# Kernel optimization log

Measured on AMD Instinct MI355X. Metric: run time of the kernel, lower is better.

Reference implementation:

```python
import jax, jax.numpy as jnp
import numpy as np

H = 16            # num_attention_heads
START_RATIO = 0.1
RECENT_RATIO = 0.4
THETA = 10000.0
CHUNK = 256       # hard-coded chunk_size in source
CLIP = 1e4        # nan_to_num posinf/neginf bound


def _rope_cos_sin(T, D, dtype):
    inv_freq = 1.0 / (THETA ** (jnp.arange(0, D, 2, dtype=jnp.float32) / D))
    freqs = jnp.arange(T, dtype=jnp.float32)[:, None] * inv_freq[None, :]  # [T, D/2]
    emb = jnp.concatenate([freqs, freqs], axis=-1)                          # [T, D]
    return jnp.cos(emb).astype(dtype), jnp.sin(emb).astype(dtype)


def _apply_rope(x, cos, sin):
    # x: [B,H,T,D]; cos/sin: [T,D] broadcast over B,H
    d = x.shape[-1] // 2
    rot = jnp.concatenate([-x[..., d:], x[..., :d]], axis=-1)
    return x * cos + rot * sin


def setup_inputs() -> dict:
    key = jax.random.key(0)
    k0, k1, k2, k3, k4 = jax.random.split(key, 5)
    B, T, Dm = 1, 2048, 2048
    scale = 1.0 / np.sqrt(Dm).astype(np.float32)
    return {
        "hidden_states": jax.random.normal(k0, (B, T, Dm), jnp.float32),
        "Wq": jax.random.normal(k1, (Dm, Dm), jnp.float32) * scale,
        "Wk": jax.random.normal(k2, (Dm, Dm), jnp.float32) * scale,
        "Wv": jax.random.normal(k3, (Dm, Dm), jnp.float32) * scale,
        "Wo": jax.random.normal(k4, (Dm, Dm), jnp.float32) * scale,
    }


def reference(hidden_states, Wq, Wk, Wv, Wo):
    B, T, Dm = hidden_states.shape
    D = Dm // H
    hs = jnp.nan_to_num(hidden_states, nan=0.0, posinf=CLIP, neginf=-CLIP)

    def proj(W):  # torch Linear: x @ W.T, then [B,T,H,D] -> [B,H,T,D]
        return (hs @ W.T).reshape(B, T, H, D).transpose(0, 2, 1, 3)

    q, k, v = proj(Wq), proj(Wk), proj(Wv)
    cos, sin = _rope_cos_sin(T, D, hs.dtype)
    q = _apply_rope(q, cos, sin)
    k = _apply_rope(k, cos, sin)

    # start+recent keep mask (past_key_value=None -> k_len == T)
    k_len = T
    sb = max(0, min(int(START_RATIO * k_len), k_len))
    rb = max(0, min(int(RECENT_RATIO * k_len), k_len - sb))
    pos = jnp.arange(k_len)
    keep = (pos < sb) | (pos >= k_len - rb)          # [K]

    MIN = jnp.finfo(hs.dtype).min
    scores = jnp.einsum('bhqd,bhkd->bhqk', q, k) / jnp.sqrt(jnp.asarray(D, hs.dtype))
    scores = jnp.where(keep, scores, MIN)
    probs = jax.nn.softmax(scores, axis=-1)          # [B,H,T,K]

    # CaM merge of evicted V into recent window, driven by the LAST query row.
    evict = k_len - rb                               # static python int
    last = probs[..., -1, :]                         # [B,H,K]
    mean_attn = last[..., evict + 1:].mean(axis=-1) + 1e-6
    p = jnp.clip(last[..., evict] / mean_attn, 0.0, 1.0)
    p = jnp.nan_to_num(p, nan=0.0, posinf=1.0, neginf=0.0)
    u = jax.random.uniform(jax.random.key(42), p.shape, p.dtype)
    bern = (u < p).astype(v.dtype)                   # [B,H]
    v_e = v[..., evict, :] * bern[..., None] / rb    # [B,H,D]
    v_merged = v.at[..., evict + 1:, :].add(v_e[..., None, :])

    # Chunked loop effect: only the last chunk's AV uses merged V.
    last_start = ((T - 1) // CHUNK) * CHUNK
    out_pre = jnp.einsum('bhqk,bhkd->bhqd', probs[:, :, :last_start], v)
    out_last = jnp.einsum('bhqk,bhkd->bhqd', probs[:, :, last_start:], v_merged)
    out = jnp.concatenate([out_pre, out_last], axis=2)   # [B,H,T,D]

    out = out.transpose(0, 2, 1, 3).reshape(B, T, Dm) @ Wo.T
    return jnp.nan_to_num(out, nan=0.0, posinf=CLIP, neginf=-CLIP)
```

## Files before the change

kernel.cpp:

```cpp
#include <hip/hip_runtime.h>
#include <stdint.h>

#define T_SEQ 2048
#define DM    2048
#define NH    16
#define HD    128
#define SB    204
#define EV    1229
#define RB    819
#define NRECF 818.0f
#define LAST_START 1792
#define SCALE 0.08838834764831845f

typedef __attribute__((ext_vector_type(8))) short short8;
typedef __attribute__((ext_vector_type(4))) short short4v;
typedef __attribute__((ext_vector_type(4))) float f32x4;

__device__ __forceinline__ unsigned short f2bf(float f) {
  uint32_t u = __float_as_uint(f);
  u += 0x7fffu + ((u >> 16) & 1u);
  return (unsigned short)(u >> 16);
}
__device__ __forceinline__ float bf2f(unsigned short s) {
  return __uint_as_float(((uint32_t)s) << 16);
}
__device__ __forceinline__ void gload16(const void* g, void* l) {
  __builtin_amdgcn_global_load_lds((const __attribute__((address_space(1))) void*)g,
                                   (__attribute__((address_space(3))) void*)l,
                                   16, 0, 0);
}
__device__ __forceinline__ float n2n(float v) {
  if (isnan(v)) return 0.0f;
  if (isinf(v)) return v > 0.0f ? 10000.0f : -10000.0f;
  return v;
}

__global__ __launch_bounds__(256) void cvt_kernel(
    const float* __restrict__ hs, const float* __restrict__ wq,
    const float* __restrict__ wk, const float* __restrict__ wv,
    const float* __restrict__ wo, unsigned short* __restrict__ hsb,
    unsigned short* __restrict__ wqb, unsigned short* __restrict__ wkb,
    unsigned short* __restrict__ wvb, unsigned short* __restrict__ wob,
    float* __restrict__ cst, float* __restrict__ snt) {
  if (blockIdx.x >= 20480) {
    int idx = (blockIdx.x - 20480) * 256 + threadIdx.x;
    int t = idx >> 6, i = idx & 63;
    float inv = (float)exp(-(double)i * log(10000.0) / 64.0);
    float ang = (float)t * inv;
    cst[idx] = (float)cos((double)ang);
    snt[idx] = (float)sin((double)ang);
    return;
  }
  int gid = blockIdx.x * 256 + threadIdx.x;
  int region = gid >> 20;
  int off4 = (gid & 1048575) * 4;
  const float* src; unsigned short* dst;
  switch (region) {
    case 0: src = hs; dst = hsb; break;
    case 1: src = wq; dst = wqb; break;
    case 2: src = wk; dst = wkb; break;
    case 3: src = wv; dst = wvb; break;
    default: src = wo; dst = wob; break;
  }
  float4 v = *(const float4*)(src + off4);
  if (region == 0) { v.x = n2n(v.x); v.y = n2n(v.y); v.z = n2n(v.z); v.w = n2n(v.w); }
  ushort4 o;
  o.x = f2bf(v.x); o.y = f2bf(v.y); o.z = f2bf(v.z); o.w = f2bf(v.w);
  *(ushort4*)(dst + off4) = o;
}

__device__ __forceinline__ void gemm_mainloop64_db(
    const unsigned short* __restrict__ A, const unsigned short* __restrict__ B,
    unsigned short* LDSBUF,
    int m0, int n0, int k0, int ksteps, int tid, f32x4 (&acc)[4][4]) {
  int w = tid >> 6, lane = tid & 63;
  int wm = w >> 1, wn = w & 1;
  int q4 = lane >> 4, r = lane & 15;
  f32x4 zero = {0.f, 0.f, 0.f, 0.f};
  #pragma unroll
  for (int mi = 0; mi < 4; mi++)
    #pragma unroll
    for (int ni = 0; ni < 4; ni++) acc[mi][ni] = zero;
  int srow = w * 32 + (lane >> 3);
  int swz = ((lane & 7) ^ (lane >> 3)) * 16;
  const char* Ag = (const char*)(A + (size_t)(m0 + srow) * DM) + swz + k0 * 2;
  const char* Bg = (const char*)(B + (size_t)(n0 + srow) * DM) + swz + k0 * 2;
  unsigned short* AsB[2] = {LDSBUF + w * 2048, LDSBUF + 16384 + w * 2048};
  unsigned short* BsB[2] = {LDSBUF + 8192 + w * 2048, LDSBUF + 24576 + w * 2048};
  #pragma unroll
  for (int g = 0; g < 4; g++) {
    gload16(Ag + g * (8 * DM * 2), AsB[0] + g * 512);
    gload16(Bg + g * (8 * DM * 2), BsB[0] + g * 512);
  }
  for (int s = 0; s < ksteps; s++) {
    int db = s & 1;
    __syncthreads();
    if (s + 1 < ksteps) {
      #pragma unroll
      for (int g = 0; g < 4; g++) {
        gload16(Ag + 128 + g * (8 * DM * 2), AsB[db ^ 1] + g * 512);
        gload16(Bg + 128 + g * (8 * DM * 2), BsB[db ^ 1] + g * 512);
      }
    }
    Ag += 128; Bg += 128;
    const unsigned short* As = LDSBUF + (db ? 16384 : 0);
    const unsigned short* Bs = LDSBUF + (db ? 24576 : 8192);
    #pragma unroll
    for (int kh = 0; kh < 2; kh++) {
      int pcs = ((kh * 4 + q4) ^ (r & 7)) * 8;
      short8 a[4], b[4];
      #pragma unroll
      for (int mi = 0; mi < 4; mi++)
        a[mi] = *(const short8*)(As + (wm * 64 + mi * 16 + r) * 64 + pcs);
      #pragma unroll
      for (int ni = 0; ni < 4; ni++)
        b[ni] = *(const short8*)(Bs + ((ni & 1) * 64 + wn * 32 + (ni >> 1) * 16 + r) * 64 + pcs);
      #pragma unroll
      for (int mi = 0; mi < 4; mi++)
        #pragma unroll
        for (int ni = 0; ni < 4; ni++)
          acc[mi][ni] = __builtin_amdgcn_mfma_f32_16x16x32_bf16(a[mi], b[ni], acc[mi][ni], 0, 0, 0);
    }
  }
}

__global__ __launch_bounds__(256, 2) void gemm_qkv_kernel(
    const unsigned short* __restrict__ hsb, const unsigned short* __restrict__ wqb,
    const unsigned short* __restrict__ wkb, const unsigned short* __restrict__ wvb,
    const float* __restrict__ cst, const float* __restrict__ snt,
    unsigned short* __restrict__ qbf, unsigned short* __restrict__ kbf,
    unsigned short* __restrict__ vbT) {
  __shared__ __align__(16) unsigned short LDSBUF[32768];
  int z = blockIdx.z;
  const unsigned short* B = (z == 0) ? wqb : (z == 1) ? wkb : wvb;
  int m0 = blockIdx.y * 128, n0 = blockIdx.x * 128;
  f32x4 acc[4][4];
  gemm_mainloop64_db(hsb, B, LDSBUF, m0, n0, 0, DM / 64, threadIdx.x, acc);
  int tid = threadIdx.x, w = tid >> 6, lane = tid & 63;
  int wm = w >> 1, wn = w & 1, q4 = lane >> 4, r = lane & 15;
  int h = n0 >> 7;
  if (z < 2) {
    unsigned short* dst = (z == 0) ? qbf : kbf;
    #pragma unroll
    for (int mi = 0; mi < 4; mi++)
      #pragma unroll
      for (int p = 0; p < 2; p++) {
        int d = wn * 32 + p * 16 + r;
        #pragma unroll
        for (int g = 0; g < 4; g++) {
          int t = m0 + wm * 64 + mi * 16 + q4 * 4 + g;
          float c = cst[t * 64 + d], s = snt[t * 64 + d];
          float x0 = acc[mi][2 * p][g], x1 = acc[mi][2 * p + 1][g];
          dst[((size_t)h * T_SEQ + t) * HD + d]      = f2bf(x0 * c - x1 * s);
          dst[((size_t)h * T_SEQ + t) * HD + d + 64] = f2bf(x1 * c + x0 * s);
        }
      }
  } else {
    __syncthreads();
    #pragma unroll
    for (int mi = 0; mi < 4; mi++)
      #pragma unroll
      for (int ni = 0; ni < 4; ni++) {
        int c = (ni & 1) * 64 + wn * 32 + (ni >> 1) * 16 + r;
        int tl = wm * 64 + mi * 16 + q4 * 4;
        short4v pv;
        pv[0] = (short)f2bf(acc[mi][ni][0]);
        pv[1] = (short)f2bf(acc[mi][ni][1]);
        pv[2] = (short)f2bf(acc[mi][ni][2]);
        pv[3] = (short)f2bf(acc[mi][ni][3]);
        *(short4v*)(LDSBUF + c * 136 + tl) = pv;
      }
    __syncthreads();
    int d = tid >> 1, th = tid & 1;
    unsigned short* gdst = vbT + ((size_t)h * HD + d) * T_SEQ + m0 + th * 64;
    const unsigned short* lsrc = LDSBUF + d * 136 + th * 64;
    #pragma unroll
    for (int j = 0; j < 8; j++)
      *(short8*)(gdst + j * 8) = *(const short8*)(lsrc + j * 8);
  }
}

__device__ __forceinline__ void attn_body(
    int kb, const unsigned short* Kt, const unsigned short* Vt,
    const unsigned short* indv, unsigned short* Psw,
    const short8 (&aq)[4], f32x4 (&o)[8], f32x4& o9, float (&evf)[4],
    int q4, int r) {
  f32x4 zero = {0.f, 0.f, 0.f, 0.f};
  int rsw = (r >> 1) & 3;
  f32x4 s0 = zero, s1 = zero;
  #pragma unroll
  for (int c = 0; c < 4; c++) {
    int pc = ((c * 4 + q4) ^ r) * 8;
    short8 bk0 = *(const short8*)(Kt + r * 128 + pc);
    short8 bk1 = *(const short8*)(Kt + (16 + r) * 128 + pc);
    s0 = __builtin_amdgcn_mfma_f32_16x16x32_bf16(aq[c], bk0, s0, 0, 0, 0);
    s1 = __builtin_amdgcn_mfma_f32_16x16x32_bf16(aq[c], bk1, s1, 0, 0, 0);
  }
  int kg0 = kb + r, kg1 = kb + 16 + r;
  bool keep0 = (kg0 < SB) || (kg0 >= EV);
  bool keep1 = (kg1 < SB) || (kg1 >= EV);
  #pragma unroll
  for (int g = 0; g < 4; g++) {
    float p0 = keep0 ? __expf(fmaf(s0[g], SCALE, -8.0f)) : 0.0f;
    float p1 = keep1 ? __expf(fmaf(s1[g], SCALE, -8.0f)) : 0.0f;
    if (kb == 1216 && kg0 == EV) evf[g] = p0;
    int row = q4 * 4 + g;
    int psw = (row >> 1) & 3;
    Psw[row * 32 + (((r >> 3) ^ psw) * 8) + (r & 7)]       = f2bf(p0);
    Psw[row * 32 + ((((r >> 3) + 2) ^ psw) * 8) + (r & 7)] = f2bf(p1);
  }
  short8 pa = *(const short8*)(Psw + r * 32 + (q4 ^ rsw) * 8);
  #pragma unroll
  for (int ni = 0; ni < 8; ni++) {
    short8 bv = *(const short8*)(Vt + (ni * 16 + r) * 32 + (q4 ^ rsw) * 8);
    o[ni] = __builtin_amdgcn_mfma_f32_16x16x32_bf16(pa, bv, o[ni], 0, 0, 0);
  }
  short8 bind = *(const short8*)(indv + r * 32 + (q4 ^ rsw) * 8);
  o9 = __builtin_amdgcn_mfma_f32_16x16x32_bf16(pa, bind, o9, 0, 0, 0);
}

__global__ __launch_bounds__(256, 2) void attn_kernel(
    const unsigned short* __restrict__ qbf, const unsigned short* __restrict__ kbf,
    const unsigned short* __restrict__ vbT, unsigned short* __restrict__ atb,
    float* __restrict__ attnf_s, float* __restrict__ Ssum, float* __restrict__ lst) {
  __shared__ __align__(16) unsigned short KtS[2][2][4096];
  __shared__ __align__(16) unsigned short VtS[2][2][4096];
  __shared__ __align__(16) unsigned short Ps[4][512];
  __shared__ __align__(16) unsigned short Ind[3 * 512];
  int tid = threadIdx.x, w = tid >> 6, lane = tid & 63;
  int q4 = lane >> 4, r = lane & 15;
  int h = blockIdx.y;
  int qb = blockIdx.x * 64 + w * 16;

  for (int idx = tid; idx < 3 * 512; idx += 256) {
    int v = idx >> 9, n = (idx >> 5) & 15, j = idx & 31;
    float val = 0.f;
    if (n == 0) val = 1.f;
    else if (n == 1) val = (v == 1) ? (j >= 14 ? 1.f : 0.f) : (v == 2 ? 1.f : 0.f);
    Ind[v * 512 + n * 32 + (((j >> 3) ^ ((n >> 1) & 3)) * 8) + (j & 7)] = f2bf(val);
  }

  short8 aq[4];
  {
    const unsigned short* qrow = qbf + ((size_t)h * T_SEQ + qb + r) * HD;
    #pragma unroll
    for (int c = 0; c < 4; c++) aq[c] = *(const short8*)(qrow + c * 32 + q4 * 8);
  }
  f32x4 zero = {0.f, 0.f, 0.f, 0.f};
  f32x4 o[8], o9;
  #pragma unroll
  for (int ni = 0; ni < 8; ni++) o[ni] = zero;
  o9 = zero;
  float evf[4] = {0.f, 0.f, 0.f, 0.f};

  const char* Kbase = (const char*)(kbf + (size_t)h * T_SEQ * HD);
  int krow0 = w * 8 + q4, krow1 = krow0 + 4;
  const char* Kg0 = Kbase + krow0 * 256 + ((r ^ (krow0 & 15)) * 16);
  const char* Kg1 = Kbase + krow1 * 256 + ((r ^ (krow1 & 15)) * 16);
  const char* Vbase = (const char*)(vbT + (size_t)h * HD * T_SEQ);
  int vsrc = ((lane & 3) ^ ((lane >> 3) & 3)) * 16;
  const char* Vg0 = Vbase + (size_t)(w * 32 + (lane >> 2)) * 4096 + vsrc;
  const char* Vg1 = Vg0 + 16 * 4096;

  auto issue_chunk = [&](int ci, int db) {
    int kb = (ci < 4) ? ci * 64 : 1216 + (ci - 4) * 64;
    gload16(Kg0 + kb * 256,         &KtS[db][0][w * 1024]);
    gload16(Kg1 + kb * 256,         &KtS[db][0][w * 1024 + 512]);
    gload16(Kg0 + (kb + 32) * 256,  &KtS[db][1][w * 1024]);
    gload16(Kg1 + (kb + 32) * 256,  &KtS[db][1][w * 1024 + 512]);
    gload16(Vg0 + kb * 2,           &VtS[db][0][w * 1024]);
    gload16(Vg1 + kb * 2,           &VtS[db][0][w * 1024 + 512]);
    gload16(Vg0 + (kb + 32) * 2,    &VtS[db][1][w * 1024]);
    gload16(Vg1 + (kb + 32) * 2,    &VtS[db][1][w * 1024 + 512]);
  };

  issue_chunk(0, 0);
  for (int ci = 0; ci < 17; ci++) {
    int db = ci & 1;
    int kb = (ci < 4) ? ci * 64 : 1216 + (ci - 4) * 64;
    const unsigned short* indA = Ind + ((ci < 4) ? 0 : (ci == 4) ? 512 : 1024);
    const unsigned short* indB = Ind + ((ci < 4) ? 0 : 1024);
    __syncthreads();
    if (ci < 16) issue_chunk(ci + 1, db ^ 1);
    attn_body(kb,      KtS[db][0], VtS[db][0], indA, &Ps[w][0], aq, o, o9, evf, q4, r);
    attn_body(kb + 32, KtS[db][1], VtS[db][1], indB, &Ps[w][0], aq, o, o9, evf, q4, r);
  }

  float invl[4], srn[4], evn[4];
  #pragma unroll
  for (int g = 0; g < 4; g++) {
    float l  = __shfl(o9[g], lane & 48, 64);
    float sr = __shfl(o9[g], (lane & 48) | 1, 64);
    float ev = __shfl(evf[g], (lane & 48) | 13, 64);
    invl[g] = 1.0f / l;
    srn[g] = sr * invl[g];
    evn[g] = ev * invl[g];
  }
  if (blockIdx.x < (LAST_START / 64)) {
    #pragma unroll
    for (int ni = 0; ni < 8; ni++)
      #pragma unroll
      for (int g = 0; g < 4; g++)
        atb[(size_t)(qb + q4 * 4 + g) * DM + h * HD + ni * 16 + r] = f2bf(o[ni][g] * invl[g]);
  } else {
    #pragma unroll
    for (int ni = 0; ni < 8; ni++)
      #pragma unroll
      for (int g = 0; g < 4; g++)
        attnf_s[(size_t)(qb - LAST_START + q4 * 4 + g) * DM + h * HD + ni * 16 + r] = o[ni][g] * invl[g];
  }
  if (r == 0) {
    #pragma unroll
    for (int g = 0; g < 4; g++) {
      int t = qb + q4 * 4 + g;
      if (t >= LAST_START) Ssum[h * 256 + (t - LAST_START)] = srn[g];
      if (t == T_SEQ - 1) { lst[h * 2] = evn[g]; lst[h * 2 + 1] = srn[g]; }
    }
  }
}

__device__ __forceinline__ void tf_round(uint32_t& x0, uint32_t& x1, int rot) {
  x0 += x1;
  x1 = (x1 << rot) | (x1 >> (32 - rot));
  x1 ^= x0;
}
__device__ __forceinline__ float bern_scale(int hh, const float* lst) {
  const uint32_t k0 = 0u, k1 = 42u, k2 = 0x1BD11BDAu ^ k0 ^ k1;
  uint32_t x0 = (uint32_t)(hh & 7), x1 = (uint32_t)((hh & 7) + 8);
  x0 += k0; x1 += k1;
  tf_round(x0, x1, 13); tf_round(x0, x1, 15); tf_round(x0, x1, 26); tf_round(x0, x1, 6);
  x0 += k1; x1 += k2 + 1u;
  tf_round(x0, x1, 17); tf_round(x0, x1, 29); tf_round(x0, x1, 16); tf_round(x0, x1, 24);
  x0 += k2; x1 += k0 + 2u;
  tf_round(x0, x1, 13); tf_round(x0, x1, 15); tf_round(x0, x1, 26); tf_round(x0, x1, 6);
  x0 += k0; x1 += k1 + 3u;
  tf_round(x0, x1, 17); tf_round(x0, x1, 29); tf_round(x0, x1, 16); tf_round(x0, x1, 24);
  x0 += k1; x1 += k2 + 4u;
  tf_round(x0, x1, 13); tf_round(x0, x1, 15); tf_round(x0, x1, 26); tf_round(x0, x1, 6);
  x0 += k2; x1 += k0 + 5u;
  uint32_t bits = (hh < 8) ? x0 : x1;
  float u = __uint_as_float((bits >> 9) | 0x3f800000u) - 1.0f;
  float evp = lst[hh * 2], srp = lst[hh * 2 + 1];
  float mean = srp * (1.0f / NRECF) + 1e-6f;
  float p = evp / mean;
  p = fminf(fmaxf(p, 0.0f), 1.0f);
  if (!(p == p)) p = 0.0f;
  return (u < p) ? (1.0f / (float)RB) : 0.0f;
}

__global__ __launch_bounds__(256) void fixup_kernel(
    const float* __restrict__ attnf_s, const float* __restrict__ Ssum,
    const float* __restrict__ lst, const unsigned short* __restrict__ vbT,
    unsigned short* __restrict__ atb) {
  int idx = blockIdx.x * 256 + threadIdx.x;
  int t2 = idx >> 11, n = idx & 2047;
  int h = n >> 7, d = n & 127;
  float bsc = bern_scale(h, lst);
  float v = attnf_s[idx];
  v += Ssum[h * 256 + t2] * bsc * bf2f(vbT[((size_t)h * HD + d) * T_SEQ + EV]);
  atb[(size_t)(t2 + LAST_START) * DM + n] = f2bf(v);
}

__global__ __launch_bounds__(256, 2) void gemm_out_kernel(
    const unsigned short* __restrict__ atb, const unsigned short* __restrict__ wob,
    float* __restrict__ part0, float* __restrict__ part1) {
  __shared__ __align__(16) unsigned short LDSBUF[32768];
  int m0 = blockIdx.y * 128, n0 = blockIdx.x * 128;
  int kz = blockIdx.z;
  float* part = kz ? part1 : part0;
  f32x4 acc[4][4];
  gemm_mainloop64_db(atb, wob, LDSBUF, m0, n0, kz * 1024, 16, threadIdx.x, acc);
  int tid = threadIdx.x, w = tid >> 6, lane = tid & 63;
  int wm = w >> 1, wn = w & 1, q4 = lane >> 4, r = lane & 15;
  #pragma unroll
  for (int mi = 0; mi < 4; mi++)
    #pragma unroll
    for (int ni = 0; ni < 4; ni++) {
      int c = n0 + (ni & 1) * 64 + wn * 32 + (ni >> 1) * 16 + r;
      #pragma unroll
      for (int g = 0; g < 4; g++) {
        int t = m0 + wm * 64 + mi * 16 + q4 * 4 + g;
        part[(size_t)t * DM + c] = acc[mi][ni][g];
      }
    }
}

__global__ __launch_bounds__(256) void add_kernel(
    const float* __restrict__ p0, const float* __restrict__ p1, float* __restrict__ out) {
  int i4 = (blockIdx.x * 256 + threadIdx.x) * 4;
  float4 a = *(const float4*)(p0 + i4);
  float4 b = *(const float4*)(p1 + i4);
  float4 o;
  o.x = n2n(a.x + b.x); o.y = n2n(a.y + b.y);
  o.z = n2n(a.z + b.z); o.w = n2n(a.w + b.w);
  *(float4*)(out + i4) = o;
}

extern "C" void kernel_launch(void* const* d_in, const int* in_sizes, int n_in,
                              void* d_out, int out_size, void* d_ws, size_t ws_size,
                              hipStream_t stream) {
  const float* hs = (const float*)d_in[0];
  const float* Wq = (const float*)d_in[1];
  const float* Wk = (const float*)d_in[2];
  const float* Wv = (const float*)d_in[3];
  const float* Wo = (const float*)d_in[4];
  char* ws = (char*)d_ws;
  const size_t MB = 1024 * 1024;
  unsigned short* hsb = (unsigned short*)(ws + 0);
  unsigned short* wqb = (unsigned short*)(ws + 8 * MB);
  unsigned short* wkb = (unsigned short*)(ws + 16 * MB);
  unsigned short* wvb = (unsigned short*)(ws + 24 * MB);
  unsigned short* wob = (unsigned short*)(ws + 32 * MB);
  unsigned short* qbf = (unsigned short*)(ws + 40 * MB);
  unsigned short* kbf = (unsigned short*)(ws + 48 * MB);
  unsigned short* vbT = (unsigned short*)(ws + 56 * MB);
  unsigned short* atb = (unsigned short*)(ws + 64 * MB);
  float* attnf_s = (float*)(ws + 72 * MB);
  float* part0 = (float*)(ws + 74 * MB);
  float* part1 = (float*)(ws + 90 * MB);
  float* cst = (float*)(ws + 106 * MB);
  float* snt = (float*)(ws + 106 * MB + 524288);
  float* Ssum = (float*)(ws + 107 * MB);
  float* lst = (float*)(ws + 107 * MB + 16384);

  cvt_kernel<<<20992, 256, 0, stream>>>(hs, Wq, Wk, Wv, Wo, hsb, wqb, wkb, wvb, wob, cst, snt);
  gemm_qkv_kernel<<<dim3(16, 16, 3), 256, 0, stream>>>(hsb, wqb, wkb, wvb, cst, snt, qbf, kbf, vbT);
  attn_kernel<<<dim3(32, 16), 256, 0, stream>>>(qbf, kbf, vbT, atb, attnf_s, Ssum, lst);
  fixup_kernel<<<2048, 256, 0, stream>>>(attnf_s, Ssum, lst, vbT, atb);
  gemm_out_kernel<<<dim3(16, 16, 2), 256, 0, stream>>>(atb, wob, part0, part1);
  add_kernel<<<4096, 256, 0, stream>>>(part0, part1, (float*)d_out);
}
```

Measured before the change: 248.2 us.

## Skip K/V projection rows for evicted keys and single-buffer GEMM LDS

The QKV projection grid now computes only the K and V row tiles that the start+recent mask can touch (the first 2 and the last 7 of 16 tiles), while Q keeps all 16. This cuts about a third of the projection GEMM work. Both GEMMs also drop LDS double-buffering in favour of one buffer with two barriers per k-step. That halves LDS use so launch bounds can allow three blocks per CU, at the cost of losing load/compute overlap inside a block. The skipped K/V rows are left unwritten, so this relies on the attention kernel never reading them, including the evict row 1229, which falls in tile 9.

Result: faster. 242.5 us (-2.3%).

```diff
diff --git a/kernel.cpp b/kernel.cpp
--- a/kernel.cpp
+++ b/kernel.cpp
@@ -69,10 +69,10 @@
   *(ushort4*)(dst + off4) = o;
 }
 
-__device__ __forceinline__ void gemm_mainloop64_db(
+__device__ __forceinline__ void gemm_mainloop64(
     const unsigned short* __restrict__ A, const unsigned short* __restrict__ B,
-    unsigned short* LDSBUF,
-    int m0, int n0, int k0, int ksteps, int tid, f32x4 (&acc)[4][4]) {
+    unsigned short* As, unsigned short* Bs, int m0, int n0, int k0, int ksteps,
+    int tid, f32x4 (&acc)[4][4]) {
   int w = tid >> 6, lane = tid & 63;
   int wm = w >> 1, wn = w & 1;
   int q4 = lane >> 4, r = lane & 15;
@@ -85,26 +85,17 @@
   int swz = ((lane & 7) ^ (lane >> 3)) * 16;
   const char* Ag = (const char*)(A + (size_t)(m0 + srow) * DM) + swz + k0 * 2;
   const char* Bg = (const char*)(B + (size_t)(n0 + srow) * DM) + swz + k0 * 2;
-  unsigned short* AsB[2] = {LDSBUF + w * 2048, LDSBUF + 16384 + w * 2048};
-  unsigned short* BsB[2] = {LDSBUF + 8192 + w * 2048, LDSBUF + 24576 + w * 2048};
-  #pragma unroll
-  for (int g = 0; g < 4; g++) {
-    gload16(Ag + g * (8 * DM * 2), AsB[0] + g * 512);
-    gload16(Bg + g * (8 * DM * 2), BsB[0] + g * 512);
-  }
+  unsigned short* Asl = As + w * 2048;
+  unsigned short* Bsl = Bs + w * 2048;
   for (int s = 0; s < ksteps; s++) {
-    int db = s & 1;
     __syncthreads();
-    if (s + 1 < ksteps) {
-      #pragma unroll
-      for (int g = 0; g < 4; g++) {
-        gload16(Ag + 128 + g * (8 * DM * 2), AsB[db ^ 1] + g * 512);
-        gload16(Bg + 128 + g * (8 * DM * 2), BsB[db ^ 1] + g * 512);
-      }
+    #pragma unroll
+    for (int g = 0; g < 4; g++) {
+      gload16(Ag + g * (8 * DM * 2), Asl + g * 512);
+      gload16(Bg + g * (8 * DM * 2), Bsl + g * 512);
     }
     Ag += 128; Bg += 128;
-    const unsigned short* As = LDSBUF + (db ? 16384 : 0);
-    const unsigned short* Bs = LDSBUF + (db ? 24576 : 8192);
+    __syncthreads();
     #pragma unroll
     for (int kh = 0; kh < 2; kh++) {
       int pcs = ((kh * 4 + q4) ^ (r & 7)) * 8;
@@ -124,33 +115,40 @@
   }
 }
 
-__global__ __launch_bounds__(256, 2) void gemm_qkv_kernel(
+__global__ __launch_bounds__(256, 3) void gemm_qkv_kernel(
     const unsigned short* __restrict__ hsb, const unsigned short* __restrict__ wqb,
     const unsigned short* __restrict__ wkb, const unsigned short* __restrict__ wvb,
     const float* __restrict__ cst, const float* __restrict__ snt,
     unsigned short* __restrict__ qbf, unsigned short* __restrict__ kbf,
     unsigned short* __restrict__ vbT) {
-  __shared__ __align__(16) unsigned short LDSBUF[32768];
-  int z = blockIdx.z;
+  __shared__ __align__(16) unsigned short LDSBUF[17408];
+  unsigned short* As = LDSBUF;
+  unsigned short* Bs = LDSBUF + 8192;
+  int y = blockIdx.y;
+  int z, mi;
+  if (y < 16)      { z = 0; mi = y; }
+  else if (y < 25) { z = 1; mi = y - 16; }
+  else             { z = 2; mi = y - 25; }
+  if (z) mi = (mi < 2) ? mi : mi + 7;
   const unsigned short* B = (z == 0) ? wqb : (z == 1) ? wkb : wvb;
-  int m0 = blockIdx.y * 128, n0 = blockIdx.x * 128;
+  int m0 = mi * 128, n0 = blockIdx.x * 128;
   f32x4 acc[4][4];
-  gemm_mainloop64_db(hsb, B, LDSBUF, m0, n0, 0, DM / 64, threadIdx.x, acc);
+  gemm_mainloop64(hsb, B, As, Bs, m0, n0, 0, DM / 64, threadIdx.x, acc);
   int tid = threadIdx.x, w = tid >> 6, lane = tid & 63;
   int wm = w >> 1, wn = w & 1, q4 = lane >> 4, r = lane & 15;
   int h = n0 >> 7;
   if (z < 2) {
     unsigned short* dst = (z == 0) ? qbf : kbf;
     #pragma unroll
-    for (int mi = 0; mi < 4; mi++)
+    for (int mj = 0; mj < 4; mj++)
       #pragma unroll
       for (int p = 0; p < 2; p++) {
         int d = wn * 32 + p * 16 + r;
         #pragma unroll
         for (int g = 0; g < 4; g++) {
-          int t = m0 + wm * 64 + mi * 16 + q4 * 4 + g;
+          int t = m0 + wm * 64 + mj * 16 + q4 * 4 + g;
           float c = cst[t * 64 + d], s = snt[t * 64 + d];
-          float x0 = acc[mi][2 * p][g], x1 = acc[mi][2 * p + 1][g];
+          float x0 = acc[mj][2 * p][g], x1 = acc[mj][2 * p + 1][g];
           dst[((size_t)h * T_SEQ + t) * HD + d]      = f2bf(x0 * c - x1 * s);
           dst[((size_t)h * T_SEQ + t) * HD + d + 64] = f2bf(x1 * c + x0 * s);
         }
@@ -158,16 +156,16 @@
   } else {
     __syncthreads();
     #pragma unroll
-    for (int mi = 0; mi < 4; mi++)
+    for (int mj = 0; mj < 4; mj++)
       #pragma unroll
       for (int ni = 0; ni < 4; ni++) {
         int c = (ni & 1) * 64 + wn * 32 + (ni >> 1) * 16 + r;
-        int tl = wm * 64 + mi * 16 + q4 * 4;
+        int tl = wm * 64 + mj * 16 + q4 * 4;
         short4v pv;
-        pv[0] = (short)f2bf(acc[mi][ni][0]);
-        pv[1] = (short)f2bf(acc[mi][ni][1]);
-        pv[2] = (short)f2bf(acc[mi][ni][2]);
-        pv[3] = (short)f2bf(acc[mi][ni][3]);
+        pv[0] = (short)f2bf(acc[mj][ni][0]);
+        pv[1] = (short)f2bf(acc[mj][ni][1]);
+        pv[2] = (short)f2bf(acc[mj][ni][2]);
+        pv[3] = (short)f2bf(acc[mj][ni][3]);
         *(short4v*)(LDSBUF + c * 136 + tl) = pv;
       }
     __syncthreads();
@@ -361,15 +359,17 @@
   atb[(size_t)(t2 + LAST_START) * DM + n] = f2bf(v);
 }
 
-__global__ __launch_bounds__(256, 2) void gemm_out_kernel(
+__global__ __launch_bounds__(256, 3) void gemm_out_kernel(
     const unsigned short* __restrict__ atb, const unsigned short* __restrict__ wob,
     float* __restrict__ part0, float* __restrict__ part1) {
-  __shared__ __align__(16) unsigned short LDSBUF[32768];
+  __shared__ __align__(16) unsigned short LDSBUF[16384];
+  unsigned short* As = LDSBUF;
+  unsigned short* Bs = LDSBUF + 8192;
   int m0 = blockIdx.y * 128, n0 = blockIdx.x * 128;
   int kz = blockIdx.z;
   float* part = kz ? part1 : part0;
   f32x4 acc[4][4];
-  gemm_mainloop64_db(atb, wob, LDSBUF, m0, n0, kz * 1024, 16, threadIdx.x, acc);
+  gemm_mainloop64(atb, wob, As, Bs, m0, n0, kz * 1024, 16, threadIdx.x, acc);
   int tid = threadIdx.x, w = tid >> 6, lane = tid & 63;
   int wm = w >> 1, wn = w & 1, q4 = lane >> 4, r = lane & 15;
   #pragma unroll
@@ -424,7 +424,7 @@
   float* lst = (float*)(ws + 107 * MB + 16384);
 
   cvt_kernel<<<20992, 256, 0, stream>>>(hs, Wq, Wk, Wv, Wo, hsb, wqb, wkb, wvb, wob, cst, snt);
-  gemm_qkv_kernel<<<dim3(16, 16, 3), 256, 0, stream>>>(hsb, wqb, wkb, wvb, cst, snt, qbf, kbf, vbT);
+  gemm_qkv_kernel<<<dim3(16, 34), 256, 0, stream>>>(hsb, wqb, wkb, wvb, cst, snt, qbf, kbf, vbT);
   attn_kernel<<<dim3(32, 16), 256, 0, stream>>>(qbf, kbf, vbT, atb, attnf_s, Ssum, lst);
   fixup_kernel<<<2048, 256, 0, stream>>>(attnf_s, Ssum, lst, vbT, atb);
   gemm_out_kernel<<<dim3(16, 16, 2), 256, 0, stream>>>(atb, wob, part0, part1);
```
